# Kernel optimization log

Hardware: AMD Instinct MI355X
Metric: run time of the kernel (lower is better)

Reference implementation:

```python
import jax, jax.numpy as jnp
import numpy as np

S = 4096            # num tokens (single causal sequence)
HID = 1024          # hidden_size
NH = 16             # num query heads
NKV = 4             # num kv heads
HD = 64             # head_dim
THETA = 10000.0
Q_SIZE = NH * HD
KV_SIZE = NKV * HD


def setup_inputs() -> dict:
    key = jax.random.key(0)
    k1, k2, k3 = jax.random.split(key, 3)
    return {
        "positions": jnp.arange(S, dtype=jnp.int32),
        "hidden_states": jax.random.normal(k1, (S, 2 * HID), dtype=jnp.float32),
        "w_qkv": jax.random.normal(k2, (Q_SIZE + 2 * KV_SIZE, 2 * HID), dtype=jnp.float32) * 0.02,
        "w_o": jax.random.normal(k3, (HID, Q_SIZE), dtype=jnp.float32) * 0.02,
    }


def _rope(x, positions):
    # x: [S, H, HD]; neox-style rotate-half RoPE
    half = HD // 2
    inv_freq = 1.0 / (THETA ** (jnp.arange(0, half, dtype=jnp.float32) / half))
    freqs = positions.astype(jnp.float32)[:, None] * inv_freq  # [S, half]
    cos = jnp.cos(freqs)[:, None, :]  # [S, 1, half]
    sin = jnp.sin(freqs)[:, None, :]
    x1, x2 = x[..., :half], x[..., half:]
    return jnp.concatenate([x1 * cos - x2 * sin, x2 * cos + x1 * sin], axis=-1)


def reference(positions, hidden_states, w_qkv, w_o):
    qkv = hidden_states @ w_qkv.T  # [S, Q_SIZE + 2*KV_SIZE]
    q = qkv[:, :Q_SIZE].reshape(S, NH, HD)
    k = qkv[:, Q_SIZE:Q_SIZE + KV_SIZE].reshape(S, NKV, HD)
    v = qkv[:, Q_SIZE + KV_SIZE:].reshape(S, NKV, HD)
    q = _rope(q, positions)
    k = _rope(k, positions)
    # GQA: group query heads over kv heads
    g = NH // NKV
    qg = q.reshape(S, NKV, g, HD)
    scale = HD ** -0.5
    scores = jnp.einsum("qhgd,thd->hgqt", qg, k) * scale  # [NKV, g, S, S]
    causal = positions[:, None] >= positions[None, :]      # [S, S]
    scores = jnp.where(causal[None, None], scores, jnp.finfo(scores.dtype).min)
    probs = jax.nn.softmax(scores, axis=-1)
    o = jnp.einsum("hgqt,thd->qhgd", probs, v).reshape(S, Q_SIZE)
    return o @ w_o.T  # [S, HID]
```

## Files before the change

### kernel.cpp

```cpp
#include <hip/hip_runtime.h>
#include <math.h>

#define S_LEN   4096
#define NHEADS  16
#define NKVH    4
#define HDIM    64
#define QKV_N   1536
#define HID2    2048
#define OUT_N   1024

typedef __attribute__((ext_vector_type(8))) __bf16 bf16x8;
typedef __attribute__((ext_vector_type(4))) __bf16 bf16x4;
typedef __attribute__((ext_vector_type(4))) float  f32x4;

#define GL_LDS16(gaddr, laddr)                                                  \
  __builtin_amdgcn_global_load_lds(                                             \
      (const __attribute__((address_space(1))) unsigned int*)(gaddr),           \
      (__attribute__((address_space(3))) unsigned int*)(laddr), 16, 0, 0)

__global__ __launch_bounds__(256) void cvt_all(const float* __restrict__ hid,
                                               const float* __restrict__ wq,
                                               const float* __restrict__ wo,
                                               __bf16* __restrict__ hid_bf,
                                               __bf16* __restrict__ wq_bf,
                                               __bf16* __restrict__ wo_bf) {
  const int n1 = S_LEN * HID2;
  const int n2 = QKV_N * HID2;
  int i = (blockIdx.x * blockDim.x + threadIdx.x) * 8;
  const float* src; __bf16* dst; int off;
  if (i < n1)           { src = hid; dst = hid_bf; off = i; }
  else if (i < n1 + n2) { src = wq;  dst = wq_bf;  off = i - n1; }
  else                  { src = wo;  dst = wo_bf;  off = i - n1 - n2; }
  float4 a = *(const float4*)(src + off);
  float4 b = *(const float4*)(src + off + 4);
  bf16x8 o = {(__bf16)a.x,(__bf16)a.y,(__bf16)a.z,(__bf16)a.w,
              (__bf16)b.x,(__bf16)b.y,(__bf16)b.z,(__bf16)b.w};
  *(bf16x8*)(dst + off) = o;
}

__global__ __launch_bounds__(256) void rope_table(const int* __restrict__ positions,
                                                  float* __restrict__ ct,
                                                  float* __restrict__ st) {
  int i = blockIdx.x * blockDim.x + threadIdx.x;
  int s = i >> 5, d = i & 31;
  double inv = pow(10000.0, -(double)d / 32.0);
  double fr = (double)positions[s] * inv;
  ct[i] = (float)cos(fr);
  st[i] = (float)sin(fr);
}

template<int BM, bool C_BF16>
__global__ __launch_bounds__(256) void gemm_m97(const __bf16* __restrict__ A,
                                                const __bf16* __restrict__ B,
                                                void* __restrict__ Cp,
                                                int M, int N, int K) {
  constexpr int TM = BM / 32;
  __shared__ __align__(16) __bf16 As[BM * 32];
  __shared__ __align__(16) __bf16 Bs[128 * 32];
  const int tid  = threadIdx.x;
  const int bm   = blockIdx.x, bn = blockIdx.y;
  const int wave = tid >> 6, lane = tid & 63;
  const int quad = lane >> 4, col = lane & 15;
  const int wm = (wave >> 1) * (BM / 2), wn = (wave & 1) * 64;

  const int lrow = lane >> 2, lcol = (lane & 3) * 8;
  const __bf16* Ag = A + (size_t)(bm * BM + wave * (BM / 4) + lrow) * K + lcol;
  const __bf16* Bg = B + (size_t)(bn * 128 + wave * 32 + lrow) * K + lcol;
  __bf16* AsW = As + wave * (BM / 4) * 32;
  __bf16* BsW = Bs + wave * 32 * 32;

  f32x4 acc[TM][4];
#pragma unroll
  for (int i = 0; i < TM; ++i)
#pragma unroll
    for (int j = 0; j < 4; ++j) acc[i][j] = (f32x4){0.f, 0.f, 0.f, 0.f};

  for (int kk = 0; kk < K; kk += 32) {
    __syncthreads();
#pragma unroll
    for (int u = 0; u < BM / 64; ++u)
      GL_LDS16(Ag + kk + (size_t)(u * 16) * K, AsW + u * 16 * 32);
    GL_LDS16(Bg + kk,                  BsW);
    GL_LDS16(Bg + kk + (size_t)16 * K, BsW + 16 * 32);
    __syncthreads();

    bf16x8 a[TM], b[4];
#pragma unroll
    for (int tm = 0; tm < TM; ++tm)
      a[tm] = *(const bf16x8*)&As[(wm + tm * 16 + col) * 32 + quad * 8];
#pragma unroll
    for (int tn = 0; tn < 4; ++tn)
      b[tn] = *(const bf16x8*)&Bs[(wn + tn * 16 + col) * 32 + quad * 8];
#pragma unroll
    for (int tm = 0; tm < TM; ++tm)
#pragma unroll
      for (int tn = 0; tn < 4; ++tn)
        acc[tm][tn] = __builtin_amdgcn_mfma_f32_16x16x32_bf16(a[tm], b[tn], acc[tm][tn], 0, 0, 0);
  }

#pragma unroll
  for (int tm = 0; tm < TM; ++tm)
#pragma unroll
    for (int tn = 0; tn < 4; ++tn) {
      int row = bm * BM + wm + tm * 16 + quad * 4;
      int cg  = bn * 128 + wn + tn * 16 + col;
#pragma unroll
      for (int r = 0; r < 4; ++r) {
        if constexpr (C_BF16)
          ((__bf16*)Cp)[(size_t)(row + r) * N + cg] = (__bf16)acc[tm][tn][r];
        else
          ((float*)Cp)[(size_t)(row + r) * N + cg] = acc[tm][tn][r];
      }
    }
}

__global__ __launch_bounds__(256) void rope_cast(const __bf16* __restrict__ qkv,
                                                 const float* __restrict__ ct,
                                                 const float* __restrict__ st,
                                                 __bf16* __restrict__ qb,
                                                 __bf16* __restrict__ kb) {
  int g = blockIdx.x * blockDim.x + threadIdx.x;
  int d = g & 31;
  int rem = g >> 5;
  int head = rem % 20;
  int s = rem / 20;
  bool isq = head < NHEADS;
  const __bf16* src = qkv + (size_t)s * QKV_N + (isq ? head * 64 : 1024 + (head - 16) * 64);
  float c  = ct[s * 32 + d];
  float sn = st[s * 32 + d];
  float x1 = (float)src[d], x2 = (float)src[d + 32];
  float y1 = x1 * c - x2 * sn;
  float y2 = x2 * c + x1 * sn;
  float scl = isq ? 0.125f : 1.0f;
  __bf16* dst = isq ? (qb + (size_t)s * 1024 + head * 64)
                    : (kb + (size_t)s * 256 + (head - 16) * 64);
  dst[d]      = (__bf16)(y1 * scl);
  dst[d + 32] = (__bf16)(y2 * scl);
}

__global__ __launch_bounds__(256) void v_transpose(const __bf16* __restrict__ qkv,
                                                   __bf16* __restrict__ vT) {
  __shared__ __align__(16) __bf16 Ts[64][72];
  const int sb = blockIdx.x, kvh = blockIdx.y, t = threadIdx.x;
  const int r = t >> 2, c16 = (t & 3) * 16;
  const __bf16* src = qkv + (size_t)(sb * 64 + r) * QKV_N + 1280 + kvh * 64 + c16;
  bf16x8 v0 = *(const bf16x8*)src;
  bf16x8 v1 = *(const bf16x8*)(src + 8);
#pragma unroll
  for (int u = 0; u < 8; ++u) {
    Ts[c16 + u][r]     = v0[u];
    Ts[c16 + 8 + u][r] = v1[u];
  }
  __syncthreads();
  __bf16* dst = vT + ((size_t)kvh * 64 + r) * S_LEN + sb * 64 + c16;
  *(bf16x8*)dst       = *(const bf16x8*)&Ts[r][c16];
  *(bf16x8*)(dst + 8) = *(const bf16x8*)&Ts[r][c16 + 8];
}

__global__ __launch_bounds__(256) void attn_split(const __bf16* __restrict__ qg,
                                                  const __bf16* __restrict__ kg,
                                                  const __bf16* __restrict__ vg,
                                                  __bf16* __restrict__ op0,
                                                  __bf16* __restrict__ op1,
                                                  float* __restrict__ lp) {
  __shared__ __align__(16) __bf16 lds[26624];
  __bf16* Qs = lds;
  __bf16* Ks = lds + 8192;
  __bf16* Vs = lds + 17408;

  const int tid = threadIdx.x;
  const int h = blockIdx.x;
  const int yy = blockIdx.y;
  const int qq = yy >> 1, split = yy & 1;
  const int qb = (qq < 16) ? qq : 47 - qq;
  const int kvh = h >> 2;
  const int wave = tid >> 6, lane = tid & 63;
  const int quad = lane >> 4, col = lane & 15;
  const int quad4 = quad * 4;
  const int qbase = qb * 128 + wave * 32;
  const int kt0 = split * (qb + 1);
  const int ktEnd = kt0 + qb + 1;

  {
    const int r = tid >> 1, c = (tid & 1) * 32;
    const __bf16* src = qg + (size_t)(qb * 128 + r) * 1024 + h * 64 + c;
    *(bf16x8*)&Qs[r * 64 + c]      = *(const bf16x8*)(src);
    *(bf16x8*)&Qs[r * 64 + c + 8]  = *(const bf16x8*)(src + 8);
    *(bf16x8*)&Qs[r * 64 + c + 16] = *(const bf16x8*)(src + 16);
    *(bf16x8*)&Qs[r * 64 + c + 24] = *(const bf16x8*)(src + 24);
  }

  const int sr = tid >> 2, sc = (tid & 3) * 16;
  const __bf16* kptr = kg + (size_t)sr * 256 + kvh * 64 + sc;
  const __bf16* vptr = vg + ((size_t)kvh * 64 + sr) * S_LEN + sc;
  bf16x8 kr0 = *(const bf16x8*)(kptr + (size_t)kt0 * 64 * 256);
  bf16x8 kr1 = *(const bf16x8*)(kptr + (size_t)kt0 * 64 * 256 + 8);
  bf16x8 vr0 = *(const bf16x8*)(vptr + (size_t)kt0 * 64);
  bf16x8 vr1 = *(const bf16x8*)(vptr + (size_t)kt0 * 64 + 8);

  __syncthreads();

  bf16x8 qf[2][2];
#pragma unroll
  for (int nq = 0; nq < 2; ++nq)
#pragma unroll
    for (int ks = 0; ks < 2; ++ks)
      qf[nq][ks] = *(const bf16x8*)&Qs[(wave * 32 + nq * 16 + col) * 64 + ks * 32 + quad * 8];

  __bf16* Pw = Qs + wave * 2048;

  f32x4 o[2][4];
  float lacc[2] = {0.f, 0.f};
#pragma unroll
  for (int i = 0; i < 2; ++i)
#pragma unroll
    for (int j = 0; j < 4; ++j) o[i][j] = (f32x4){0.f, 0.f, 0.f, 0.f};

  for (int kt = kt0; kt < ktEnd; ++kt) {
    const int cur = (kt - kt0) & 1;
    {
      __bf16* kd = Ks + cur * 4608 + sr * 72 + sc;
      *(bf16x8*)kd       = kr0;
      *(bf16x8*)(kd + 8) = kr1;
      __bf16* vd = Vs + cur * 4608 + sr * 72 + sc;
      *(bf16x8*)vd       = vr0;
      *(bf16x8*)(vd + 8) = vr1;
    }
    if (kt + 1 < ktEnd) {
      const __bf16* kn = kptr + (size_t)(kt + 1) * 64 * 256;
      const __bf16* vn = vptr + (size_t)(kt + 1) * 64;
      kr0 = *(const bf16x8*)(kn);
      kr1 = *(const bf16x8*)(kn + 8);
      vr0 = *(const bf16x8*)(vn);
      vr1 = *(const bf16x8*)(vn + 8);
    }
    __syncthreads();

    if (kt * 64 > qbase + 31) continue;

    f32x4 sf[4][2];
#pragma unroll
    for (int mt = 0; mt < 4; ++mt)
#pragma unroll
      for (int nq = 0; nq < 2; ++nq) sf[mt][nq] = (f32x4){0.f, 0.f, 0.f, 0.f};
#pragma unroll
    for (int ks = 0; ks < 2; ++ks) {
      bf16x8 kf[4];
#pragma unroll
      for (int mt = 0; mt < 4; ++mt)
        kf[mt] = *(const bf16x8*)&Ks[cur * 4608 + (mt * 16 + col) * 72 + ks * 32 + quad * 8];
#pragma unroll
      for (int mt = 0; mt < 4; ++mt)
#pragma unroll
        for (int nq = 0; nq < 2; ++nq)
          sf[mt][nq] = __builtin_amdgcn_mfma_f32_16x16x32_bf16(kf[mt], qf[nq][ks], sf[mt][nq], 0, 0, 0);
    }

    const bool full = (kt * 64 + 63 <= qbase);
#pragma unroll
    for (int mt = 0; mt < 4; ++mt) {
      const int tb = mt * 16 + quad4;
#pragma unroll
      for (int nq = 0; nq < 2; ++nq) {
        const int thr = qbase + nq * 16 + col - kt * 64;
        float p0 = __expf(sf[mt][nq][0]);
        float p1 = __expf(sf[mt][nq][1]);
        float p2 = __expf(sf[mt][nq][2]);
        float p3 = __expf(sf[mt][nq][3]);
        if (!full) {
          if (tb + 0 > thr) p0 = 0.f;
          if (tb + 1 > thr) p1 = 0.f;
          if (tb + 2 > thr) p2 = 0.f;
          if (tb + 3 > thr) p3 = 0.f;
        }
        lacc[nq] += (p0 + p1) + (p2 + p3);
        const int g = ((mt * 2 + (quad >> 1)) ^ (col & 7));
        bf16x4 pk = {(__bf16)p0, (__bf16)p1, (__bf16)p2, (__bf16)p3};
        *(bf16x4*)&Pw[(nq * 16 + col) * 64 + g * 8 + (quad & 1) * 4] = pk;
      }
    }

#pragma unroll
    for (int ks = 0; ks < 2; ++ks) {
      bf16x8 pf[2], vf[4];
#pragma unroll
      for (int mq = 0; mq < 2; ++mq)
        pf[mq] = *(const bf16x8*)&Pw[(mq * 16 + col) * 64 + (((ks * 4 + quad) ^ (col & 7)) * 8)];
#pragma unroll
      for (int nd = 0; nd < 4; ++nd)
        vf[nd] = *(const bf16x8*)&Vs[cur * 4608 + (nd * 16 + col) * 72 + ks * 32 + quad * 8];
#pragma unroll
      for (int mq = 0; mq < 2; ++mq)
#pragma unroll
        for (int nd = 0; nd < 4; ++nd)
          o[mq][nd] = __builtin_amdgcn_mfma_f32_16x16x32_bf16(pf[mq], vf[nd], o[mq][nd], 0, 0, 0);
    }
  }

#pragma unroll
  for (int nq = 0; nq < 2; ++nq) {
    lacc[nq] += __shfl_xor(lacc[nq], 16, 64);
    lacc[nq] += __shfl_xor(lacc[nq], 32, 64);
  }
  __syncthreads();
  float* lsh = (float*)Pw;
  if (lane < 16) { lsh[lane] = lacc[0]; lsh[16 + lane] = lacc[1]; }
  __syncthreads();

  __bf16* op = split ? op1 : op0;
#pragma unroll
  for (int mq = 0; mq < 2; ++mq)
#pragma unroll
    for (int r = 0; r < 4; ++r) {
      float l = lsh[mq * 16 + quad4 + r];
      float linv = (l > 0.f) ? 1.f / l : 0.f;
      int row = qb * 128 + wave * 32 + mq * 16 + quad4 + r;
#pragma unroll
      for (int nd = 0; nd < 4; ++nd)
        op[(size_t)row * 1024 + h * 64 + nd * 16 + col] =
            (__bf16)(o[mq][nd][r] * linv);
    }
  if (col == 0) {
#pragma unroll
    for (int mq = 0; mq < 2; ++mq)
#pragma unroll
      for (int r = 0; r < 4; ++r)
        lp[(size_t)(split * S_LEN + qb * 128 + wave * 32 + mq * 16 + quad4 + r) * NHEADS + h] =
            lsh[mq * 16 + quad4 + r];
  }
}

__global__ __launch_bounds__(256) void attn_combine(const __bf16* __restrict__ op0,
                                                    const __bf16* __restrict__ op1,
                                                    const float* __restrict__ lp,
                                                    __bf16* __restrict__ ob) {
  int i = blockIdx.x * 256 + threadIdx.x;
  int row = i >> 7, c8 = (i & 127) * 8;
  int h = c8 >> 6;
  float l0 = lp[(size_t)row * NHEADS + h];
  float l1 = lp[(size_t)(S_LEN + row) * NHEADS + h];
  float inv = 1.f / (l0 + l1);
  float w0 = l0 * inv, w1 = l1 * inv;
  bf16x8 a = *(const bf16x8*)(op0 + (size_t)row * 1024 + c8);
  bf16x8 b = *(const bf16x8*)(op1 + (size_t)row * 1024 + c8);
  bf16x8 o;
#pragma unroll
  for (int u = 0; u < 8; ++u)
    o[u] = (__bf16)((float)a[u] * w0 + (float)b[u] * w1);
  *(bf16x8*)(ob + (size_t)row * 1024 + c8) = o;
}

extern "C" void kernel_launch(void* const* d_in, const int* in_sizes, int n_in,
                              void* d_out, int out_size, void* d_ws, size_t ws_size,
                              hipStream_t stream) {
  const int*   positions = (const int*)d_in[0];
  const float* hidden    = (const float*)d_in[1];
  const float* w_qkv     = (const float*)d_in[2];
  const float* w_o       = (const float*)d_in[3];
  float* out = (float*)d_out;

  char* ws = (char*)d_ws;
  __bf16* qkv_bf  = (__bf16*)ws;
  __bf16* Opart0  = (__bf16*)ws;
  __bf16* attn_bf = (__bf16*)ws;
  __bf16* hid_bf  = (__bf16*)(ws + 12582912);
  __bf16* q_bf    = (__bf16*)(ws + 12582912);
  __bf16* k_bf    = (__bf16*)(ws + 20971520);
  __bf16* vT      = (__bf16*)(ws + 23068672);
  float*  ct      = (float*)(ws + 29360128);
  float*  st      = (float*)(ws + 29884416);
  float*  lpart   = (float*)(ws + 29360128);
  __bf16* wq_bf   = (__bf16*)(ws + 30408704);
  __bf16* Opart1  = (__bf16*)(ws + 30408704);
  __bf16* wo_bf   = (__bf16*)(ws + 38797312);

  cvt_all<<<(S_LEN * HID2 + QKV_N * HID2 + OUT_N * OUT_N) / 8 / 256, 256, 0, stream>>>(
      hidden, w_qkv, w_o, hid_bf, wq_bf, wo_bf);
  rope_table<<<S_LEN * 32 / 256, 256, 0, stream>>>(positions, ct, st);

  gemm_m97<64, true><<<dim3(S_LEN / 64, QKV_N / 128), 256, 0, stream>>>(
      hid_bf, wq_bf, qkv_bf, S_LEN, QKV_N, HID2);

  rope_cast<<<(S_LEN * 20 * 32) / 256, 256, 0, stream>>>(qkv_bf, ct, st, q_bf, k_bf);
  v_transpose<<<dim3(S_LEN / 64, NKVH), 256, 0, stream>>>(qkv_bf, vT);

  attn_split<<<dim3(NHEADS, 64), 256, 0, stream>>>(q_bf, k_bf, vT, Opart0, Opart1, lpart);
  attn_combine<<<S_LEN * 128 / 256, 256, 0, stream>>>(Opart0, Opart1, lpart, attn_bf);

  gemm_m97<64, false><<<dim3(S_LEN / 64, OUT_N / 128), 256, 0, stream>>>(
      attn_bf, wo_bf, out, S_LEN, OUT_N, OUT_N);
}
```

Baseline: 238.0 us.

## Switch attention to 32x32x16 MFMA with register-resident P via permlane swap

```diff
diff --git a/kernel.cpp b/kernel.cpp
--- a/kernel.cpp
+++ b/kernel.cpp
@@ -12,11 +12,19 @@
 typedef __attribute__((ext_vector_type(8))) __bf16 bf16x8;
 typedef __attribute__((ext_vector_type(4))) __bf16 bf16x4;
 typedef __attribute__((ext_vector_type(4))) float  f32x4;
+typedef __attribute__((ext_vector_type(16))) float f32x16;
+typedef __attribute__((ext_vector_type(4))) unsigned int u32x4;
 
 #define GL_LDS16(gaddr, laddr)                                                  \
   __builtin_amdgcn_global_load_lds(                                             \
       (const __attribute__((address_space(1))) unsigned int*)(gaddr),           \
       (__attribute__((address_space(3))) unsigned int*)(laddr), 16, 0, 0)
+
+__device__ __forceinline__ unsigned cvt_pk_bf16(float lo, float hi) {
+  unsigned r;
+  asm("v_cvt_pk_bf16_f32 %0, %1, %2" : "=v"(r) : "v"(lo), "v"(hi));
+  return r;
+}
 
 __global__ __launch_bounds__(256) void cvt_all(const float* __restrict__ hid,
                                                const float* __restrict__ wq,
@@ -157,16 +165,15 @@
   *(bf16x8*)(dst + 8) = *(const bf16x8*)&Ts[r][c16 + 8];
 }
 
-__global__ __launch_bounds__(256) void attn_split(const __bf16* __restrict__ qg,
-                                                  const __bf16* __restrict__ kg,
-                                                  const __bf16* __restrict__ vg,
-                                                  __bf16* __restrict__ op0,
-                                                  __bf16* __restrict__ op1,
-                                                  float* __restrict__ lp) {
-  __shared__ __align__(16) __bf16 lds[26624];
-  __bf16* Qs = lds;
-  __bf16* Ks = lds + 8192;
-  __bf16* Vs = lds + 17408;
+__global__ __launch_bounds__(256, 4) void attn_split(const __bf16* __restrict__ qg,
+                                                     const __bf16* __restrict__ kg,
+                                                     const __bf16* __restrict__ vg,
+                                                     __bf16* __restrict__ op0,
+                                                     __bf16* __restrict__ op1,
+                                                     float* __restrict__ lp) {
+  __shared__ __align__(16) __bf16 lds[18432];
+  __bf16* Ks = lds;
+  __bf16* Vs = lds + 9216;
 
   const int tid = threadIdx.x;
   const int h = blockIdx.x;
@@ -175,8 +182,8 @@
   const int qb = (qq < 16) ? qq : 47 - qq;
   const int kvh = h >> 2;
   const int wave = tid >> 6, lane = tid & 63;
-  const int quad = lane >> 4, col = lane & 15;
-  const int quad4 = quad * 4;
+  const int r31 = lane & 31, hi = lane >> 5;
+  const int hi4 = hi * 4, hi8 = hi * 8;
   const int qbase = qb * 128 + wave * 32;
   const int kt0 = split * (qb + 1);
   const int ktEnd = kt0 + qb + 1;
@@ -184,10 +191,11 @@
   {
     const int r = tid >> 1, c = (tid & 1) * 32;
     const __bf16* src = qg + (size_t)(qb * 128 + r) * 1024 + h * 64 + c;
-    *(bf16x8*)&Qs[r * 64 + c]      = *(const bf16x8*)(src);
-    *(bf16x8*)&Qs[r * 64 + c + 8]  = *(const bf16x8*)(src + 8);
-    *(bf16x8*)&Qs[r * 64 + c + 16] = *(const bf16x8*)(src + 16);
-    *(bf16x8*)&Qs[r * 64 + c + 24] = *(const bf16x8*)(src + 24);
+    __bf16* dq = lds + r * 72 + c;
+    *(bf16x8*)(dq)      = *(const bf16x8*)(src);
+    *(bf16x8*)(dq + 8)  = *(const bf16x8*)(src + 8);
+    *(bf16x8*)(dq + 16) = *(const bf16x8*)(src + 16);
+    *(bf16x8*)(dq + 24) = *(const bf16x8*)(src + 24);
   }
 
   const int sr = tid >> 2, sc = (tid & 3) * 16;
@@ -200,21 +208,19 @@
 
   __syncthreads();
 
-  bf16x8 qf[2][2];
-#pragma unroll
-  for (int nq = 0; nq < 2; ++nq)
-#pragma unroll
-    for (int ks = 0; ks < 2; ++ks)
-      qf[nq][ks] = *(const bf16x8*)&Qs[(wave * 32 + nq * 16 + col) * 64 + ks * 32 + quad * 8];
-
-  __bf16* Pw = Qs + wave * 2048;
-
-  f32x4 o[2][4];
-  float lacc[2] = {0.f, 0.f};
-#pragma unroll
-  for (int i = 0; i < 2; ++i)
-#pragma unroll
-    for (int j = 0; j < 4; ++j) o[i][j] = (f32x4){0.f, 0.f, 0.f, 0.f};
+  bf16x8 qf[4];
+#pragma unroll
+  for (int dc = 0; dc < 4; ++dc)
+    qf[dc] = *(const bf16x8*)&lds[(wave * 32 + r31) * 72 + dc * 16 + hi8];
+
+  __syncthreads();
+
+  f32x16 o[2];
+#pragma unroll
+  for (int dt = 0; dt < 2; ++dt)
+#pragma unroll
+    for (int g = 0; g < 16; ++g) o[dt][g] = 0.f;
+  float lacc = 0.f;
 
   for (int kt = kt0; kt < ktEnd; ++kt) {
     const int cur = (kt - kt0) & 1;
@@ -238,96 +244,73 @@
 
     if (kt * 64 > qbase + 31) continue;
 
-    f32x4 sf[4][2];
-#pragma unroll
-    for (int mt = 0; mt < 4; ++mt)
-#pragma unroll
-      for (int nq = 0; nq < 2; ++nq) sf[mt][nq] = (f32x4){0.f, 0.f, 0.f, 0.f};
-#pragma unroll
-    for (int ks = 0; ks < 2; ++ks) {
-      bf16x8 kf[4];
-#pragma unroll
-      for (int mt = 0; mt < 4; ++mt)
-        kf[mt] = *(const bf16x8*)&Ks[cur * 4608 + (mt * 16 + col) * 72 + ks * 32 + quad * 8];
-#pragma unroll
-      for (int mt = 0; mt < 4; ++mt)
-#pragma unroll
-        for (int nq = 0; nq < 2; ++nq)
-          sf[mt][nq] = __builtin_amdgcn_mfma_f32_16x16x32_bf16(kf[mt], qf[nq][ks], sf[mt][nq], 0, 0, 0);
+    const bool full = (kt * 64 + 63 <= qbase);
+    const int thr = qbase + r31 - kt * 64;
+
+    bf16x8 pa[4];
+#pragma unroll
+    for (int kb = 0; kb < 2; ++kb) {
+      f32x16 sf;
+#pragma unroll
+      for (int g = 0; g < 16; ++g) sf[g] = 0.f;
+#pragma unroll
+      for (int dc = 0; dc < 4; ++dc) {
+        bf16x8 kf = *(const bf16x8*)&Ks[cur * 4608 + (kb * 32 + r31) * 72 + dc * 16 + hi8];
+        sf = __builtin_amdgcn_mfma_f32_32x32x16_bf16(kf, qf[dc], sf, 0, 0, 0);
+      }
+      float p[16];
+#pragma unroll
+      for (int g = 0; g < 16; ++g) {
+        float e = __expf(sf[g]);
+        if (!full) {
+          const int krow = kb * 32 + (g & 3) + 8 * (g >> 2) + hi4;
+          if (krow > thr) e = 0.f;
+        }
+        p[g] = e;
+      }
+#pragma unroll
+      for (int m = 0; m < 4; ++m)
+        lacc += (p[4 * m] + p[4 * m + 1]) + (p[4 * m + 2] + p[4 * m + 3]);
+#pragma unroll
+      for (int half = 0; half < 2; ++half) {
+        unsigned a0 = cvt_pk_bf16(p[8 * half + 0], p[8 * half + 1]);
+        unsigned a1 = cvt_pk_bf16(p[8 * half + 2], p[8 * half + 3]);
+        unsigned b0 = cvt_pk_bf16(p[8 * half + 4], p[8 * half + 5]);
+        unsigned b1 = cvt_pk_bf16(p[8 * half + 6], p[8 * half + 7]);
+        asm("v_permlane32_swap_b32 %0, %1" : "+v"(a0), "+v"(b0));
+        asm("v_permlane32_swap_b32 %0, %1" : "+v"(a1), "+v"(b1));
+        u32x4 t = {a0, a1, b0, b1};
+        pa[kb * 2 + half] = __builtin_bit_cast(bf16x8, t);
+      }
     }
 
-    const bool full = (kt * 64 + 63 <= qbase);
-#pragma unroll
-    for (int mt = 0; mt < 4; ++mt) {
-      const int tb = mt * 16 + quad4;
-#pragma unroll
-      for (int nq = 0; nq < 2; ++nq) {
-        const int thr = qbase + nq * 16 + col - kt * 64;
-        float p0 = __expf(sf[mt][nq][0]);
-        float p1 = __expf(sf[mt][nq][1]);
-        float p2 = __expf(sf[mt][nq][2]);
-        float p3 = __expf(sf[mt][nq][3]);
-        if (!full) {
-          if (tb + 0 > thr) p0 = 0.f;
-          if (tb + 1 > thr) p1 = 0.f;
-          if (tb + 2 > thr) p2 = 0.f;
-          if (tb + 3 > thr) p3 = 0.f;
-        }
-        lacc[nq] += (p0 + p1) + (p2 + p3);
-        const int g = ((mt * 2 + (quad >> 1)) ^ (col & 7));
-        bf16x4 pk = {(__bf16)p0, (__bf16)p1, (__bf16)p2, (__bf16)p3};
-        *(bf16x4*)&Pw[(nq * 16 + col) * 64 + g * 8 + (quad & 1) * 4] = pk;
-      }
-    }
-
-#pragma unroll
-    for (int ks = 0; ks < 2; ++ks) {
-      bf16x8 pf[2], vf[4];
-#pragma unroll
-      for (int mq = 0; mq < 2; ++mq)
-        pf[mq] = *(const bf16x8*)&Pw[(mq * 16 + col) * 64 + (((ks * 4 + quad) ^ (col & 7)) * 8)];
-#pragma unroll
-      for (int nd = 0; nd < 4; ++nd)
-        vf[nd] = *(const bf16x8*)&Vs[cur * 4608 + (nd * 16 + col) * 72 + ks * 32 + quad * 8];
-#pragma unroll
-      for (int mq = 0; mq < 2; ++mq)
-#pragma unroll
-        for (int nd = 0; nd < 4; ++nd)
-          o[mq][nd] = __builtin_amdgcn_mfma_f32_16x16x32_bf16(pf[mq], vf[nd], o[mq][nd], 0, 0, 0);
-    }
-  }
-
-#pragma unroll
-  for (int nq = 0; nq < 2; ++nq) {
-    lacc[nq] += __shfl_xor(lacc[nq], 16, 64);
-    lacc[nq] += __shfl_xor(lacc[nq], 32, 64);
-  }
+#pragma unroll
+    for (int dt = 0; dt < 2; ++dt)
+#pragma unroll
+      for (int kc = 0; kc < 4; ++kc) {
+        bf16x8 vf = *(const bf16x8*)&Vs[cur * 4608 + (dt * 32 + r31) * 72 + kc * 16 + hi8];
+        o[dt] = __builtin_amdgcn_mfma_f32_32x32x16_bf16(pa[kc], vf, o[dt], 0, 0, 0);
+      }
+  }
+
+  lacc += __shfl_xor(lacc, 32, 64);
   __syncthreads();
-  float* lsh = (float*)Pw;
-  if (lane < 16) { lsh[lane] = lacc[0]; lsh[16 + lane] = lacc[1]; }
-  __syncthreads();
+  float* lshw = (float*)lds + wave * 32;
+  if (lane < 32) lshw[lane] = lacc;
+  asm volatile("s_waitcnt lgkmcnt(0)" ::: "memory");
 
   __bf16* op = split ? op1 : op0;
 #pragma unroll
-  for (int mq = 0; mq < 2; ++mq)
-#pragma unroll
-    for (int r = 0; r < 4; ++r) {
-      float l = lsh[mq * 16 + quad4 + r];
-      float linv = (l > 0.f) ? 1.f / l : 0.f;
-      int row = qb * 128 + wave * 32 + mq * 16 + quad4 + r;
-#pragma unroll
-      for (int nd = 0; nd < 4; ++nd)
-        op[(size_t)row * 1024 + h * 64 + nd * 16 + col] =
-            (__bf16)(o[mq][nd][r] * linv);
-    }
-  if (col == 0) {
-#pragma unroll
-    for (int mq = 0; mq < 2; ++mq)
-#pragma unroll
-      for (int r = 0; r < 4; ++r)
-        lp[(size_t)(split * S_LEN + qb * 128 + wave * 32 + mq * 16 + quad4 + r) * NHEADS + h] =
-            lsh[mq * 16 + quad4 + r];
-  }
+  for (int g = 0; g < 16; ++g) {
+    const int rl = (g & 3) + 8 * (g >> 2) + hi4;
+    float l = lshw[rl];
+    float linv = (l > 0.f) ? 1.f / l : 0.f;
+    const size_t row = (size_t)(qb * 128 + wave * 32 + rl);
+    op[row * 1024 + h * 64 + r31]      = (__bf16)(o[0][g] * linv);
+    op[row * 1024 + h * 64 + 32 + r31] = (__bf16)(o[1][g] * linv);
+  }
+  if (lane < 32)
+    lp[(size_t)(split * S_LEN + qb * 128 + wave * 32 + lane) * NHEADS + h] = lacc;
 }
 
 __global__ __launch_bounds__(256) void attn_combine(const __bf16* __restrict__ op0,
```

After: 228.3 us. 1.04x faster.
